# Performance work log

Measured on AMD Instinct MI355X. Metric: run time of the kernel, lower is better.

Reference implementation:

```python
import jax, jax.numpy as jnp
import numpy as np

D_MODEL = 512
HEADS = 8
D_FF = 1024
EPS = 1e-5


def layer_norm(x, gamma, beta):
    mu = jnp.mean(x, axis=-1, keepdims=True)
    var = jnp.mean(jnp.square(x - mu), axis=-1, keepdims=True)
    return (x - mu) * jax.lax.rsqrt(var + EPS) * gamma + beta


def mha(q, k, v, mask=None):
    # q,k,v: [B, S, D]; no input/output projections in the original module
    B, Sq, D = q.shape
    Sk = k.shape[1]
    dk = D // HEADS
    qh = q.reshape(B, Sq, HEADS, dk).transpose(0, 2, 1, 3)  # [B,H,Sq,dk]
    kh = k.reshape(B, Sk, HEADS, dk).transpose(0, 2, 1, 3)
    vh = v.reshape(B, Sk, HEADS, dk).transpose(0, 2, 1, 3)
    scores = jnp.einsum('bhqd,bhkd->bhqk', qh, kh) / np.sqrt(dk).astype(q.dtype)
    if mask is not None:
        scores = jnp.where(mask == 0, jnp.asarray(-1e9, scores.dtype), scores)
    attn = jax.nn.softmax(scores, axis=-1)  # dropout is identity in eval mode
    out = jnp.einsum('bhqk,bhkd->bhqd', attn, vh)
    return out.transpose(0, 2, 1, 3).reshape(B, Sq, D)


def setup_inputs() -> dict:
    key = jax.random.key(0)
    ks = jax.random.split(key, 8)
    B, S = 4, 2048
    x = jax.random.normal(ks[0], (B, S, D_MODEL), dtype=jnp.float32)
    encoder_output = jax.random.normal(ks[1], (B, S, D_MODEL), dtype=jnp.float32)
    mask = jax.random.randint(ks[2], (B, 1, S, S), 0, 2, dtype=jnp.int32)
    params = {
        'ln1_g': jnp.ones((D_MODEL,), jnp.float32), 'ln1_b': jnp.zeros((D_MODEL,), jnp.float32),
        'ln2_g': jnp.ones((D_MODEL,), jnp.float32), 'ln2_b': jnp.zeros((D_MODEL,), jnp.float32),
        'ln3_g': jnp.ones((D_MODEL,), jnp.float32), 'ln3_b': jnp.zeros((D_MODEL,), jnp.float32),
        'W1': jax.random.normal(ks[3], (D_MODEL, D_FF), jnp.float32) * (1.0 / np.sqrt(D_MODEL)),
        'b1': jnp.zeros((D_FF,), jnp.float32),
        'W2': jax.random.normal(ks[4], (D_FF, D_MODEL), jnp.float32) * (1.0 / np.sqrt(D_FF)),
        'b2': jnp.zeros((D_MODEL,), jnp.float32),
    }
    return {'x': x, 'encoder_output': encoder_output, 'mask': mask, **params}


def reference(x, encoder_output, mask, ln1_g, ln1_b, ln2_g, ln2_b, ln3_g, ln3_b, W1, b1, W2, b2):
    # pre-norm masked self-attention + residual (dropout = identity, eval mode)
    x1 = layer_norm(x, ln1_g, ln1_b)
    x = x + mha(x1, x1, x1, mask)
    # pre-norm cross-attention + residual
    x1 = layer_norm(x, ln2_g, ln2_b)
    x = x + mha(x1, encoder_output, encoder_output, None)
    # pre-norm FFN + residual
    x1 = layer_norm(x, ln3_g, ln3_b)
    h = jax.nn.relu(x1 @ W1 + b1)
    x = x + (h @ W2 + b2)
    return x
```

## Files before the change

### kernel.cpp

```cpp
#include <hip/hip_runtime.h>
#include <hip/hip_bf16.h>

#define D_MODEL 512
#define HEADS   8
#define DK      64
#define D_FF    1024
#define SEQ     2048
#define BATCH   4
#define NTOK    (BATCH*SEQ)
#define NELEM   (NTOK*D_MODEL)

#define QSCALE  0.18033688011112042f
#define MFIX    40.0f

typedef __attribute__((ext_vector_type(8))) short bf8_t;
typedef __attribute__((ext_vector_type(4))) float f4_t;

#define GLD16(gp, lp) __builtin_amdgcn_global_load_lds( \
    (const __attribute__((address_space(1))) void*)(gp), \
    (__attribute__((address_space(3))) void*)(lp), 16, 0, 0)

__device__ __forceinline__ float ldf(const void* p, size_t i, int f32) {
    return f32 ? ((const float*)p)[i] : __bfloat162float(((const __hip_bfloat16*)p)[i]);
}
__device__ __forceinline__ short f2bf(float f) {
    union { __hip_bfloat16 h; short s; } u; u.h = __float2bfloat16(f); return u.s;
}
__device__ __forceinline__ float bf2f(short s) {
    return __uint_as_float(((unsigned)(unsigned short)s) << 16);
}
__device__ __forceinline__ unsigned fbits(float f) { return __float_as_uint(f); }

__device__ __forceinline__ float fast_exp2(float x) {
    float r; asm("v_exp_f32 %0, %1" : "=v"(r) : "v"(x)); return r;
}

__global__ void detect_k(const uint4* __restrict__ w, int* __restrict__ flags) {
    __shared__ int found;
    if (threadIdx.x == 0) found = 0;
    __syncthreads();
    int hit = 0;
    for (int i = threadIdx.x; i < 4096; i += 256) {
        uint4 u = w[i];
        if (((u.x & 0x7F80u) == 0x7F80u) || ((u.y & 0x7F80u) == 0x7F80u) ||
            ((u.z & 0x7F80u) == 0x7F80u) || ((u.w & 0x7F80u) == 0x7F80u)) hit = 1;
    }
    if (hit) atomicOr(&found, 1);
    __syncthreads();
    if (threadIdx.x == 0) flags[0] = found ? 1 : 0;
}

__device__ __forceinline__ void transpose_body(const void* src, __hip_bfloat16* dst,
                                               int K, int N, int bxi, int byi, int f32,
                                               __hip_bfloat16 (*t)[33]) {
    int bx = bxi * 32, by = byi * 32;
    int tx = threadIdx.x & 31, ty = threadIdx.x >> 5;
    #pragma unroll
    for (int j = 0; j < 32; j += 8)
        t[ty + j][tx] = __float2bfloat16(ldf(src, (size_t)(by + ty + j) * N + bx + tx, f32));
    __syncthreads();
    #pragma unroll
    for (int j = 0; j < 32; j += 8)
        dst[(size_t)(bx + ty + j) * K + by + tx] = t[tx][ty + j];
}

__global__ __launch_bounds__(256)
void prep_k(const void* __restrict__ enc, const int* __restrict__ mask,
            const void* __restrict__ W1, const void* __restrict__ W2,
            const int* __restrict__ flagp,
            __hip_bfloat16* __restrict__ bufE, unsigned* __restrict__ mb,
            __hip_bfloat16* __restrict__ W1T, __hip_bfloat16* __restrict__ W2T) {
    __shared__ __hip_bfloat16 t[32][33];
    int f32 = *flagp;
    int bid = blockIdx.x;
    if (bid < 16384) {
        int i = bid * 256 + threadIdx.x;
        bufE[i] = __float2bfloat16(ldf(enc, i, f32));
    } else if (bid < 18432) {
        int row  = (bid - 16384) * 4 + (threadIdx.x >> 6);
        int lane = threadIdx.x & 63;
        const int* mr = mask + (size_t)row * SEQ;
        for (int it = 0; it < SEQ/64; it++) {
            unsigned long long bal = __ballot(mr[it*64 + lane] != 0);
            if (lane == 0)  mb[(size_t)row*(SEQ/32) + it*2]     = (unsigned)bal;
            if (lane == 32) mb[(size_t)row*(SEQ/32) + it*2 + 1] = (unsigned)(bal >> 32);
        }
    } else if (bid < 18944) {
        int lb = bid - 18432;
        transpose_body(W1, W1T, D_MODEL, D_FF, lb & 31, lb >> 5, f32, t);
    } else {
        int lb = bid - 18944;
        transpose_body(W2, W2T, D_FF, D_MODEL, lb & 15, lb >> 4, f32, t);
    }
}

__global__ __launch_bounds__(256)
void ln_first_k(const void* __restrict__ x, const void* __restrict__ g,
                const void* __restrict__ b, const int* __restrict__ flagp,
                float* __restrict__ xout, __hip_bfloat16* __restrict__ y) {
    int f32  = *flagp;
    int row  = blockIdx.x * 4 + (threadIdx.x >> 6);
    int lane = threadIdx.x & 63;
    size_t base = (size_t)row * D_MODEL;
    float v[8];
    float s = 0.f;
    #pragma unroll
    for (int i = 0; i < 8; i++) { v[i] = ldf(x, base + lane + i*64, f32); s += v[i]; }
    #pragma unroll
    for (int off = 32; off; off >>= 1) s += __shfl_xor(s, off);
    float mu = s * (1.f / D_MODEL);
    float ss = 0.f;
    #pragma unroll
    for (int i = 0; i < 8; i++) { float d = v[i] - mu; ss += d * d; }
    #pragma unroll
    for (int off = 32; off; off >>= 1) ss += __shfl_xor(ss, off);
    float rstd = rsqrtf(ss * (1.f / D_MODEL) + 1e-5f);
    #pragma unroll
    for (int i = 0; i < 8; i++) {
        int c = lane + i*64;
        xout[base + c] = v[i];
        y[base + c] = __float2bfloat16((v[i] - mu) * rstd * ldf(g, c, f32) + ldf(b, c, f32));
    }
}

__global__ __launch_bounds__(256)
void layernorm_k(const float* __restrict__ x, const void* __restrict__ g,
                 const void* __restrict__ b, const int* __restrict__ flagp,
                 __hip_bfloat16* __restrict__ y) {
    int f32  = *flagp;
    int row  = blockIdx.x * 4 + (threadIdx.x >> 6);
    int lane = threadIdx.x & 63;
    const float* xr = x + (size_t)row * D_MODEL;
    float v[8];
    float s = 0.f;
    #pragma unroll
    for (int i = 0; i < 8; i++) { v[i] = xr[lane + i*64]; s += v[i]; }
    #pragma unroll
    for (int off = 32; off; off >>= 1) s += __shfl_xor(s, off);
    float mu = s * (1.f / D_MODEL);
    float ss = 0.f;
    #pragma unroll
    for (int i = 0; i < 8; i++) { float d = v[i] - mu; ss += d * d; }
    #pragma unroll
    for (int off = 32; off; off >>= 1) ss += __shfl_xor(ss, off);
    float rstd = rsqrtf(ss * (1.f / D_MODEL) + 1e-5f);
    __hip_bfloat16* yr = y + (size_t)row * D_MODEL;
    #pragma unroll
    for (int i = 0; i < 8; i++) {
        int c = lane + i*64;
        yr[c] = __float2bfloat16((v[i] - mu) * rstd * ldf(g, c, f32) + ldf(b, c, f32));
    }
}

__device__ __forceinline__ bf8_t prescale_q(bf8_t q) {
    bf8_t r;
    #pragma unroll
    for (int j = 0; j < 8; j++) r[j] = f2bf(bf2f(q[j]) * QSCALE);
    return r;
}

template<bool HAS_MASK>
__global__ __launch_bounds__(256, 2)
void attn_mfma_k(const __hip_bfloat16* __restrict__ Q, const __hip_bfloat16* __restrict__ K,
                 const __hip_bfloat16* __restrict__ V, const unsigned* __restrict__ mbits,
                 float* __restrict__ Xout) {
    int bid = blockIdx.x;
    int qt = bid & 15;
    int h  = (bid >> 4) & 7;
    int b  = bid >> 7;
    int q0 = qt * 128;
    int tid  = threadIdx.x;
    int w    = tid >> 6;
    int lane = tid & 63;
    int c    = lane & 15;
    int quad = lane >> 4;

    __shared__ __hip_bfloat16 Kt[4][64 * 64];
    __shared__ __hip_bfloat16 VT[4][64 * 64];
    __shared__ __hip_bfloat16 Pb[4][2][16 * 64];

    bf8_t qf[2][2];
    #pragma unroll
    for (int g = 0; g < 2; g++) {
        const __hip_bfloat16* qrp = Q + ((size_t)(b*SEQ + q0 + 32*w + 16*g + c)) * D_MODEL + h*DK;
        qf[g][0] = prescale_q(*(const bf8_t*)(qrp + quad*8));
        qf[g][1] = prescale_q(*(const bf8_t*)(qrp + 32 + quad*8));
    }

    int kpo[4][2], vpo[4][2];
    #pragma unroll
    for (int t = 0; t < 4; t++)
        #pragma unroll
        for (int kh = 0; kh < 2; kh++) {
            int row = 16*t + c;
            kpo[t][kh] = (row*64 + (((4*kh + quad) ^ (row & 7)) * 8)) * 2;
            vpo[t][kh] = (row*64 + (((4*kh + quad) ^ (row & 7) ^ ((row >> 3) & 7)) * 8)) * 2;
        }

    int key0 = (tid >> 3) * 2, d0 = (tid & 7) * 8;
    int vtwo[8];
    #pragma unroll
    for (int j = 0; j < 8; j++) {
        int dk = d0 + j;
        int ch = (key0 >> 3) ^ (dk & 7) ^ ((dk >> 3) & 7);
        vtwo[j] = dk*128 + ch*16 + (key0 & 7)*2;
    }

    int krow[2], kc8[2];
    #pragma unroll
    for (int i = 0; i < 2; i++) {
        int idx = i*256 + tid;
        krow[i] = idx >> 3;
        kc8[i]  = ((idx & 7) ^ (krow[i] & 7)) * 8;
    }

    char* pbw[2] = { (char*)&Pb[w][0][0], (char*)&Pb[w][1][0] };
    int pwoff[4], proff[2];
    #pragma unroll
    for (int nt = 0; nt < 4; nt++)
        pwoff[nt] = c*128 + (((2*nt + (quad >> 1)) ^ (c & 7)) * 16) + (quad & 1)*8;
    #pragma unroll
    for (int kh = 0; kh < 2; kh++)
        proff[kh] = c*128 + (((4*kh + quad) ^ (c & 7)) * 16);

    const unsigned* mrp[2] = {nullptr, nullptr};
    if (HAS_MASK) {
        mrp[0] = mbits + (size_t)(b*SEQ + q0 + 32*w + c) * (SEQ/32);
        mrp[1] = mrp[0] + (size_t)16 * (SEQ/32);
    }
    int qsh = quad * 4;

    short onev = (c == 0) ? (short)0x3F80 : (short)0;
    bf8_t ones = {onev, onev, onev, onev, onev, onev, onev, onev};

    f4_t o[2][4];
    #pragma unroll
    for (int g = 0; g < 2; g++)
        #pragma unroll
        for (int mt = 0; mt < 4; mt++) o[g][mt] = (f4_t){0.f,0.f,0.f,0.f};
    f4_t l_acc[2] = {(f4_t){0.f,0.f,0.f,0.f}, (f4_t){0.f,0.f,0.f,0.f}};

    const size_t kvbase = (size_t)b * SEQ * D_MODEL + (size_t)h * DK;

    auto loadV = [&](int k0, bf8_t (&r0)[2], bf8_t (&r1)[2]) {
        #pragma unroll
        for (int t = 0; t < 2; t++) {
            const __hip_bfloat16* Vg = V + kvbase + (size_t)(k0 + t*64 + key0) * D_MODEL + d0;
            r0[t] = *(const bf8_t*)Vg;
            r1[t] = *(const bf8_t*)(Vg + D_MODEL);
        }
    };
    auto stageK = [&](int k0, int bufbase) {
        #pragma unroll
        for (int t = 0; t < 2; t++) {
            const __hip_bfloat16* Kg = K + kvbase + (size_t)(k0 + t*64) * D_MODEL;
            GLD16(Kg + (size_t)krow[0]*D_MODEL + kc8[0], (char*)&Kt[bufbase + t][0] + (w*64) * 16);
            GLD16(Kg + (size_t)krow[1]*D_MODEL + kc8[1], (char*)&Kt[bufbase + t][0] + (256 + w*64) * 16);
        }
    };
    auto writeV = [&](const bf8_t (&r0)[2], const bf8_t (&r1)[2], int bufbase) {
        #pragma unroll
        for (int t = 0; t < 2; t++) {
            const unsigned* v0u = (const unsigned*)&r0[t];
            const unsigned* v1u = (const unsigned*)&r1[t];
            char* vb = (char*)&VT[bufbase + t][0];
            #pragma unroll
            for (int dw = 0; dw < 4; dw++) {
                *(unsigned*)(vb + vtwo[2*dw])     = __builtin_amdgcn_perm(v1u[dw], v0u[dw], 0x05040100u);
                *(unsigned*)(vb + vtwo[2*dw + 1]) = __builtin_amdgcn_perm(v1u[dw], v0u[dw], 0x07060302u);
            }
        }
    };

    uint4 pm[2];
    if (HAS_MASK) { pm[0] = *(const uint4*)(mrp[0]); pm[1] = *(const uint4*)(mrp[1]); }
    bf8_t cv0[2], cv1[2];
    loadV(0, cv0, cv1);
    stageK(0, 0);
    writeV(cv0, cv1, 0);
    __syncthreads();

    for (int ph = 0; ph < SEQ/128; ph++) {
        int pb = (ph & 1) ? 2 : 0;
        int nb = pb ^ 2;

        uint4 nm[2];
        bf8_t nv0[2], nv1[2];
        if (ph < SEQ/128 - 1) {
            int kn = (ph + 1) * 128;
            if (HAS_MASK) {
                nm[0] = *(const uint4*)(mrp[0] + (kn >> 5));
                nm[1] = *(const uint4*)(mrp[1] + (kn >> 5));
            }
            loadV(kn, nv0, nv1);
            stageK(kn, nb);
        }

        #pragma unroll
        for (int t = 0; t < 2; t++) {
            const char* ktb = (const char*)&Kt[pb + t][0];
            const char* vtb = (const char*)&VT[pb + t][0];

            f4_t s[2][4];
            #pragma unroll
            for (int nt = 0; nt < 4; nt++) {
                s[0][nt] = (f4_t){-MFIX,-MFIX,-MFIX,-MFIX};
                s[1][nt] = (f4_t){-MFIX,-MFIX,-MFIX,-MFIX};
            }
            __builtin_amdgcn_s_setprio(1);
            #pragma unroll
            for (int nt = 0; nt < 4; nt++)
                #pragma unroll
                for (int kh = 0; kh < 2; kh++) {
                    bf8_t kf = *(const bf8_t*)(ktb + kpo[nt][kh]);
                    s[0][nt] = __builtin_amdgcn_mfma_f32_16x16x32_bf16(kf, qf[0][kh], s[0][nt], 0, 0, 0);
                    s[1][nt] = __builtin_amdgcn_mfma_f32_16x16x32_bf16(kf, qf[1][kh], s[1][nt], 0, 0, 0);
                }
            __builtin_amdgcn_s_setprio(0);

            #pragma unroll
            for (int g = 0; g < 2; g++) {
                unsigned wq0 = 0xffffffffu, wq1 = 0xffffffffu;
                if (HAS_MASK) {
                    wq0 = (t ? pm[g].z : pm[g].x) >> qsh;
                    wq1 = (t ? pm[g].w : pm[g].y) >> qsh;
                }
                #pragma unroll
                for (int nt = 0; nt < 4; nt++) {
                    #pragma unroll
                    for (int r = 0; r < 4; r++) {
                        float p = fast_exp2(s[g][nt][r]);
                        if (HAS_MASK) {
                            unsigned sel = (nt < 2) ? wq0 : wq1;
                            if (!((sel >> ((nt & 1)*16 + r)) & 1u)) p = 0.f;
                        }
                        s[g][nt][r] = p;
                    }
                    unsigned pk0 = __builtin_amdgcn_perm(fbits(s[g][nt][1]), fbits(s[g][nt][0]), 0x07060302u);
                    unsigned pk1 = __builtin_amdgcn_perm(fbits(s[g][nt][3]), fbits(s[g][nt][2]), 0x07060302u);
                    *(uint2*)(pbw[g] + pwoff[nt]) = make_uint2(pk0, pk1);
                }
            }

            __builtin_amdgcn_s_setprio(1);
            #pragma unroll
            for (int kh = 0; kh < 2; kh++) {
                bf8_t pfA = *(const bf8_t*)(pbw[0] + proff[kh]);
                bf8_t pfB = *(const bf8_t*)(pbw[1] + proff[kh]);
                l_acc[0] = __builtin_amdgcn_mfma_f32_16x16x32_bf16(ones, pfA, l_acc[0], 0, 0, 0);
                l_acc[1] = __builtin_amdgcn_mfma_f32_16x16x32_bf16(ones, pfB, l_acc[1], 0, 0, 0);
                #pragma unroll
                for (int mt = 0; mt < 4; mt++) {
                    bf8_t vf = *(const bf8_t*)(vtb + vpo[mt][kh]);
                    o[0][mt] = __builtin_amdgcn_mfma_f32_16x16x32_bf16(vf, pfA, o[0][mt], 0, 0, 0);
                    o[1][mt] = __builtin_amdgcn_mfma_f32_16x16x32_bf16(vf, pfB, o[1][mt], 0, 0, 0);
                }
            }
            __builtin_amdgcn_s_setprio(0);
        }

        if (ph < SEQ/128 - 1) {
            writeV(nv0, nv1, nb);
            if (HAS_MASK) { pm[0] = nm[0]; pm[1] = nm[1]; }
        }
        __syncthreads();
    }

    #pragma unroll
    for (int g = 0; g < 2; g++) {
        float lq = __shfl(l_acc[g][0], c);
        float il = 1.f / fmaxf(lq, 1e-35f);
        size_t rb = ((size_t)(b*SEQ + q0 + 32*w + 16*g + c)) * D_MODEL + h*DK;
        #pragma unroll
        for (int mt = 0; mt < 4; mt++) {
            float4* xp = (float4*)(Xout + rb + 16*mt + quad*4);
            float4 x4 = *xp;
            x4.x += o[g][mt][0] * il;
            x4.y += o[g][mt][1] * il;
            x4.z += o[g][mt][2] * il;
            x4.w += o[g][mt][3] * il;
            *xp = x4;
        }
    }
}

__global__ __launch_bounds__(256, 2)
void gemm_relu_k(const __hip_bfloat16* __restrict__ A, const __hip_bfloat16* __restrict__ BT,
                 const void* __restrict__ bias, const int* __restrict__ flagp,
                 __hip_bfloat16* __restrict__ C, int Ksz, int Nsz) {
    int f32 = *flagp;
    __shared__ __hip_bfloat16 As[128 * 64];
    __shared__ __hip_bfloat16 Bs[128 * 64];
    int tid  = threadIdx.x;
    int w    = tid >> 6;
    int c    = tid & 15;
    int quad = (tid >> 4) & 3;
    int wy = w >> 1, wx = w & 1;
    int r0 = blockIdx.y * 128, c0 = blockIdx.x * 128;

    f4_t acc[4][4];
    #pragma unroll
    for (int i = 0; i < 4; i++)
        #pragma unroll
        for (int j = 0; j < 4; j++) acc[i][j] = (f4_t){0.f,0.f,0.f,0.f};

    for (int k0 = 0; k0 < Ksz; k0 += 64) {
        __syncthreads();
        #pragma unroll
        for (int i = 0; i < 4; i++) {
            int idx = i*256 + tid;
            int row = idx >> 3, c8 = idx & 7;
            GLD16(A  + (size_t)(r0 + row) * Ksz + k0 + ((c8 ^ (row & 7)) * 8),
                  (char*)As + (size_t)(i*256 + w*64) * 16);
            GLD16(BT + (size_t)(c0 + row) * Ksz + k0 + ((c8 ^ (row & 7)) * 8),
                  (char*)Bs + (size_t)(i*256 + w*64) * 16);
        }
        __syncthreads();

        #pragma unroll
        for (int kh = 0; kh < 2; kh++) {
            bf8_t af[4], bf[4];
            #pragma unroll
            for (int mt = 0; mt < 4; mt++) {
                int row = wy*64 + mt*16 + c;
                af[mt] = *(const bf8_t*)&As[row*64 + (((kh*4 + quad) ^ (row & 7)) * 8)];
            }
            #pragma unroll
            for (int nt = 0; nt < 4; nt++) {
                int row = wx*64 + nt*16 + c;
                bf[nt] = *(const bf8_t*)&Bs[row*64 + (((kh*4 + quad) ^ (row & 7)) * 8)];
            }
            #pragma unroll
            for (int mt = 0; mt < 4; mt++)
                #pragma unroll
                for (int nt = 0; nt < 4; nt++)
                    acc[mt][nt] = __builtin_amdgcn_mfma_f32_16x16x32_bf16(af[mt], bf[nt], acc[mt][nt], 0, 0, 0);
        }
    }

    #pragma unroll
    for (int mt = 0; mt < 4; mt++)
        #pragma unroll
        for (int nt = 0; nt < 4; nt++) {
            int col = c0 + wx*64 + nt*16 + c;
            float bv = ldf(bias, col, f32);
            #pragma unroll
            for (int r = 0; r < 4; r++) {
                int m = r0 + wy*64 + mt*16 + quad*4 + r;
                C[(size_t)m * Nsz + col] = __float2bfloat16(fmaxf(acc[mt][nt][r] + bv, 0.f));
            }
        }
}

__global__ __launch_bounds__(256, 2)
void gemm_out_k(const __hip_bfloat16* __restrict__ A, const __hip_bfloat16* __restrict__ BT,
                const void* __restrict__ bias, const float* __restrict__ resid,
                const int* __restrict__ flagp, void* __restrict__ out, int Ksz, int Nsz) {
    int f32 = *flagp;
    __shared__ __hip_bfloat16 As[128 * 64];
    __shared__ __hip_bfloat16 Bs[64 * 64];
    int tid  = threadIdx.x;
    int w    = tid >> 6;
    int c    = tid & 15;
    int quad = (tid >> 4) & 3;
    int r0 = blockIdx.y * 128, c0 = blockIdx.x * 64;

    f4_t acc[2][4];
    #pragma unroll
    for (int i = 0; i < 2; i++)
        #pragma unroll
        for (int j = 0; j < 4; j++) acc[i][j] = (f4_t){0.f,0.f,0.f,0.f};

    for (int k0 = 0; k0 < Ksz; k0 += 64) {
        __syncthreads();
        #pragma unroll
        for (int i = 0; i < 4; i++) {
            int idx = i*256 + tid;
            int row = idx >> 3, c8 = idx & 7;
            GLD16(A + (size_t)(r0 + row) * Ksz + k0 + ((c8 ^ (row & 7)) * 8),
                  (char*)As + (size_t)(i*256 + w*64) * 16);
        }
        #pragma unroll
        for (int i = 0; i < 2; i++) {
            int idx = i*256 + tid;
            int row = idx >> 3, c8 = idx & 7;
            GLD16(BT + (size_t)(c0 + row) * Ksz + k0 + ((c8 ^ (row & 7)) * 8),
                  (char*)Bs + (size_t)(i*256 + w*64) * 16);
        }
        __syncthreads();

        #pragma unroll
        for (int kh = 0; kh < 2; kh++) {
            bf8_t af[2], bf[4];
            #pragma unroll
            for (int mt = 0; mt < 2; mt++) {
                int row = w*32 + mt*16 + c;
                af[mt] = *(const bf8_t*)&As[row*64 + (((kh*4 + quad) ^ (row & 7)) * 8)];
            }
            #pragma unroll
            for (int nt = 0; nt < 4; nt++) {
                int row = nt*16 + c;
                bf[nt] = *(const bf8_t*)&Bs[row*64 + (((kh*4 + quad) ^ (row & 7)) * 8)];
            }
            #pragma unroll
            for (int mt = 0; mt < 2; mt++)
                #pragma unroll
                for (int nt = 0; nt < 4; nt++)
                    acc[mt][nt] = __builtin_amdgcn_mfma_f32_16x16x32_bf16(af[mt], bf[nt], acc[mt][nt], 0, 0, 0);
        }
    }

    #pragma unroll
    for (int mt = 0; mt < 2; mt++)
        #pragma unroll
        for (int nt = 0; nt < 4; nt++) {
            int col = c0 + nt*16 + c;
            float bv = ldf(bias, col, f32);
            #pragma unroll
            for (int r = 0; r < 4; r++) {
                int m = r0 + w*32 + mt*16 + quad*4 + r;
                float v = acc[mt][nt][r] + bv + resid[(size_t)m * Nsz + col];
                if (f32) ((float*)out)[(size_t)m * Nsz + col] = v;
                else     ((__hip_bfloat16*)out)[(size_t)m * Nsz + col] = __float2bfloat16(v);
            }
        }
}

extern "C" void kernel_launch(void* const* d_in, const int* in_sizes, int n_in,
                              void* d_out, int out_size, void* d_ws, size_t ws_size,
                              hipStream_t stream) {
    const void* x    = d_in[0];
    const void* enc  = d_in[1];
    const int*  mask = (const int*)d_in[2];
    const void* ln1g = d_in[3];
    const void* ln1b = d_in[4];
    const void* ln2g = d_in[5];
    const void* ln2b = d_in[6];
    const void* ln3g = d_in[7];
    const void* ln3b = d_in[8];
    const void* W1   = d_in[9];
    const void* b1   = d_in[10];
    const void* W2   = d_in[11];
    const void* b2   = d_in[12];

    char* ws = (char*)d_ws;
    float*          bufX  = (float*)ws;
    __hip_bfloat16* bufQ  = (__hip_bfloat16*)(ws + (16u<<20));
    __hip_bfloat16* bufE  = (__hip_bfloat16*)(ws + (24u<<20));
    __hip_bfloat16* bufH  = (__hip_bfloat16*)(ws + (32u<<20));
    __hip_bfloat16* W1T   = (__hip_bfloat16*)(ws + (48u<<20));
    __hip_bfloat16* W2T   = (__hip_bfloat16*)(ws + (49u<<20));
    unsigned*       mbits = (unsigned*)(ws + (50u<<20));
    int*            flags = (int*)(ws + (52u<<20));

    dim3 blk(256);
    detect_k<<<1, blk, 0, stream>>>((const uint4*)x, flags);
    prep_k<<<19456, blk, 0, stream>>>(enc, mask, W1, W2, flags, bufE, mbits, W1T, W2T);

    ln_first_k<<<NTOK/4, blk, 0, stream>>>(x, ln1g, ln1b, flags, bufX, bufQ);
    attn_mfma_k<true><<<BATCH*HEADS*(SEQ/128), blk, 0, stream>>>(bufQ, bufQ, bufQ, mbits, bufX);
    layernorm_k<<<NTOK/4, blk, 0, stream>>>(bufX, ln2g, ln2b, flags, bufQ);
    attn_mfma_k<false><<<BATCH*HEADS*(SEQ/128), blk, 0, stream>>>(bufQ, bufE, bufE, nullptr, bufX);
    layernorm_k<<<NTOK/4, blk, 0, stream>>>(bufX, ln3g, ln3b, flags, bufQ);
    gemm_relu_k<<<dim3(D_FF/128, NTOK/128), blk, 0, stream>>>(bufQ, W1T, b1, flags, bufH, D_MODEL, D_FF);
    gemm_out_k<<<dim3(D_MODEL/64, NTOK/128), blk, 0, stream>>>(bufH, W2T, b2, bufX, flags, d_out, D_FF, D_MODEL);
}
```

Before: 343.0 us.

## Fold first layernorm into prep kernel, swizzle block order, double-buffer GEMM tiles

Moves the first layernorm into the preprocessing kernel as extra blocks, which removes one kernel launch. Remaps block indices in the attention kernels and both FFN GEMMs so neighbouring blocks are spread across the 8 XCDs, aiming for better L2 locality. The GEMMs now double-buffer their LDS tiles, so the next K-slice is fetched while the current one is computed. LDS use doubles, which may lower occupancy at the declared launch bounds.

```diff
diff --git a/kernel.cpp b/kernel.cpp
--- a/kernel.cpp
+++ b/kernel.cpp
@@ -67,9 +67,12 @@
 __global__ __launch_bounds__(256)
 void prep_k(const void* __restrict__ enc, const int* __restrict__ mask,
             const void* __restrict__ W1, const void* __restrict__ W2,
+            const void* __restrict__ x, const void* __restrict__ ln1g,
+            const void* __restrict__ ln1b,
             const int* __restrict__ flagp,
             __hip_bfloat16* __restrict__ bufE, unsigned* __restrict__ mb,
-            __hip_bfloat16* __restrict__ W1T, __hip_bfloat16* __restrict__ W2T) {
+            __hip_bfloat16* __restrict__ W1T, __hip_bfloat16* __restrict__ W2T,
+            float* __restrict__ bufX, __hip_bfloat16* __restrict__ bufQ) {
     __shared__ __hip_bfloat16 t[32][33];
     int f32 = *flagp;
     int bid = blockIdx.x;
@@ -88,38 +91,32 @@
     } else if (bid < 18944) {
         int lb = bid - 18432;
         transpose_body(W1, W1T, D_MODEL, D_FF, lb & 31, lb >> 5, f32, t);
-    } else {
+    } else if (bid < 19456) {
         int lb = bid - 18944;
         transpose_body(W2, W2T, D_FF, D_MODEL, lb & 15, lb >> 4, f32, t);
-    }
-}
-
-__global__ __launch_bounds__(256)
-void ln_first_k(const void* __restrict__ x, const void* __restrict__ g,
-                const void* __restrict__ b, const int* __restrict__ flagp,
-                float* __restrict__ xout, __hip_bfloat16* __restrict__ y) {
-    int f32  = *flagp;
-    int row  = blockIdx.x * 4 + (threadIdx.x >> 6);
-    int lane = threadIdx.x & 63;
-    size_t base = (size_t)row * D_MODEL;
-    float v[8];
-    float s = 0.f;
-    #pragma unroll
-    for (int i = 0; i < 8; i++) { v[i] = ldf(x, base + lane + i*64, f32); s += v[i]; }
-    #pragma unroll
-    for (int off = 32; off; off >>= 1) s += __shfl_xor(s, off);
-    float mu = s * (1.f / D_MODEL);
-    float ss = 0.f;
-    #pragma unroll
-    for (int i = 0; i < 8; i++) { float d = v[i] - mu; ss += d * d; }
-    #pragma unroll
-    for (int off = 32; off; off >>= 1) ss += __shfl_xor(ss, off);
-    float rstd = rsqrtf(ss * (1.f / D_MODEL) + 1e-5f);
-    #pragma unroll
-    for (int i = 0; i < 8; i++) {
-        int c = lane + i*64;
-        xout[base + c] = v[i];
-        y[base + c] = __float2bfloat16((v[i] - mu) * rstd * ldf(g, c, f32) + ldf(b, c, f32));
+    } else {
+        int row  = (bid - 19456) * 4 + (threadIdx.x >> 6);
+        int lane = threadIdx.x & 63;
+        size_t base = (size_t)row * D_MODEL;
+        float v[8];
+        float s = 0.f;
+        #pragma unroll
+        for (int i = 0; i < 8; i++) { v[i] = ldf(x, base + lane + i*64, f32); s += v[i]; }
+        #pragma unroll
+        for (int off = 32; off; off >>= 1) s += __shfl_xor(s, off);
+        float mu = s * (1.f / D_MODEL);
+        float ss = 0.f;
+        #pragma unroll
+        for (int i = 0; i < 8; i++) { float d = v[i] - mu; ss += d * d; }
+        #pragma unroll
+        for (int off = 32; off; off >>= 1) ss += __shfl_xor(ss, off);
+        float rstd = rsqrtf(ss * (1.f / D_MODEL) + 1e-5f);
+        #pragma unroll
+        for (int i = 0; i < 8; i++) {
+            int c = lane + i*64;
+            bufX[base + c] = v[i];
+            bufQ[base + c] = __float2bfloat16((v[i] - mu) * rstd * ldf(ln1g, c, f32) + ldf(ln1b, c, f32));
+        }
     }
 }
 
@@ -164,7 +161,8 @@
 void attn_mfma_k(const __hip_bfloat16* __restrict__ Q, const __hip_bfloat16* __restrict__ K,
                  const __hip_bfloat16* __restrict__ V, const unsigned* __restrict__ mbits,
                  float* __restrict__ Xout) {
-    int bid = blockIdx.x;
+    int bid0 = blockIdx.x;
+    int bid = ((bid0 & 7) << 6) | (bid0 >> 3);
     int qt = bid & 15;
     int h  = (bid >> 4) & 7;
     int b  = bid >> 7;
@@ -389,14 +387,16 @@
                  const void* __restrict__ bias, const int* __restrict__ flagp,
                  __hip_bfloat16* __restrict__ C, int Ksz, int Nsz) {
     int f32 = *flagp;
-    __shared__ __hip_bfloat16 As[128 * 64];
-    __shared__ __hip_bfloat16 Bs[128 * 64];
+    __shared__ __hip_bfloat16 As[2][128 * 64];
+    __shared__ __hip_bfloat16 Bs[2][128 * 64];
     int tid  = threadIdx.x;
     int w    = tid >> 6;
     int c    = tid & 15;
     int quad = (tid >> 4) & 3;
     int wy = w >> 1, wx = w & 1;
-    int r0 = blockIdx.y * 128, c0 = blockIdx.x * 128;
+    int lin = blockIdx.y * gridDim.x + blockIdx.x;
+    int swz = ((lin & 7) << 6) | (lin >> 3);
+    int r0 = (swz >> 3) * 128, c0 = (swz & 7) * 128;
 
     f4_t acc[4][4];
     #pragma unroll
@@ -404,18 +404,24 @@
         #pragma unroll
         for (int j = 0; j < 4; j++) acc[i][j] = (f4_t){0.f,0.f,0.f,0.f};
 
-    for (int k0 = 0; k0 < Ksz; k0 += 64) {
-        __syncthreads();
+    auto stage = [&](int k0, int bi) {
         #pragma unroll
         for (int i = 0; i < 4; i++) {
             int idx = i*256 + tid;
             int row = idx >> 3, c8 = idx & 7;
             GLD16(A  + (size_t)(r0 + row) * Ksz + k0 + ((c8 ^ (row & 7)) * 8),
-                  (char*)As + (size_t)(i*256 + w*64) * 16);
+                  (char*)&As[bi][0] + (size_t)(i*256 + w*64) * 16);
             GLD16(BT + (size_t)(c0 + row) * Ksz + k0 + ((c8 ^ (row & 7)) * 8),
-                  (char*)Bs + (size_t)(i*256 + w*64) * 16);
-        }
-        __syncthreads();
+                  (char*)&Bs[bi][0] + (size_t)(i*256 + w*64) * 16);
+        }
+    };
+
+    stage(0, 0);
+    __syncthreads();
+    int nk = Ksz >> 6;
+    for (int ks = 0; ks < nk; ks++) {
+        int bi = ks & 1;
+        if (ks + 1 < nk) stage((ks + 1) << 6, bi ^ 1);
 
         #pragma unroll
         for (int kh = 0; kh < 2; kh++) {
@@ -423,12 +429,12 @@
             #pragma unroll
             for (int mt = 0; mt < 4; mt++) {
                 int row = wy*64 + mt*16 + c;
-                af[mt] = *(const bf8_t*)&As[row*64 + (((kh*4 + quad) ^ (row & 7)) * 8)];
+                af[mt] = *(const bf8_t*)&As[bi][row*64 + (((kh*4 + quad) ^ (row & 7)) * 8)];
             }
             #pragma unroll
             for (int nt = 0; nt < 4; nt++) {
                 int row = wx*64 + nt*16 + c;
-                bf[nt] = *(const bf8_t*)&Bs[row*64 + (((kh*4 + quad) ^ (row & 7)) * 8)];
+                bf[nt] = *(const bf8_t*)&Bs[bi][row*64 + (((kh*4 + quad) ^ (row & 7)) * 8)];
             }
             #pragma unroll
             for (int mt = 0; mt < 4; mt++)
@@ -436,6 +442,7 @@
                 for (int nt = 0; nt < 4; nt++)
                     acc[mt][nt] = __builtin_amdgcn_mfma_f32_16x16x32_bf16(af[mt], bf[nt], acc[mt][nt], 0, 0, 0);
         }
+        __syncthreads();
     }
 
     #pragma unroll
@@ -457,13 +464,15 @@
                 const void* __restrict__ bias, const float* __restrict__ resid,
                 const int* __restrict__ flagp, void* __restrict__ out, int Ksz, int Nsz) {
     int f32 = *flagp;
-    __shared__ __hip_bfloat16 As[128 * 64];
-    __shared__ __hip_bfloat16 Bs[64 * 64];
+    __shared__ __hip_bfloat16 As[2][128 * 64];
+    __shared__ __hip_bfloat16 Bs[2][64 * 64];
     int tid  = threadIdx.x;
     int w    = tid >> 6;
     int c    = tid & 15;
     int quad = (tid >> 4) & 3;
-    int r0 = blockIdx.y * 128, c0 = blockIdx.x * 64;
+    int lin = blockIdx.y * gridDim.x + blockIdx.x;
+    int swz = ((lin & 7) << 6) | (lin >> 3);
+    int r0 = (swz >> 3) * 128, c0 = (swz & 7) * 64;
 
     f4_t acc[2][4];
     #pragma unroll
@@ -471,23 +480,29 @@
         #pragma unroll
         for (int j = 0; j < 4; j++) acc[i][j] = (f4_t){0.f,0.f,0.f,0.f};
 
-    for (int k0 = 0; k0 < Ksz; k0 += 64) {
-        __syncthreads();
+    auto stage = [&](int k0, int bi) {
         #pragma unroll
         for (int i = 0; i < 4; i++) {
             int idx = i*256 + tid;
             int row = idx >> 3, c8 = idx & 7;
             GLD16(A + (size_t)(r0 + row) * Ksz + k0 + ((c8 ^ (row & 7)) * 8),
-                  (char*)As + (size_t)(i*256 + w*64) * 16);
+                  (char*)&As[bi][0] + (size_t)(i*256 + w*64) * 16);
         }
         #pragma unroll
         for (int i = 0; i < 2; i++) {
             int idx = i*256 + tid;
             int row = idx >> 3, c8 = idx & 7;
             GLD16(BT + (size_t)(c0 + row) * Ksz + k0 + ((c8 ^ (row & 7)) * 8),
-                  (char*)Bs + (size_t)(i*256 + w*64) * 16);
-        }
-        __syncthreads();
+                  (char*)&Bs[bi][0] + (size_t)(i*256 + w*64) * 16);
+        }
+    };
+
+    stage(0, 0);
+    __syncthreads();
+    int nk = Ksz >> 6;
+    for (int ks = 0; ks < nk; ks++) {
+        int bi = ks & 1;
+        if (ks + 1 < nk) stage((ks + 1) << 6, bi ^ 1);
 
         #pragma unroll
         for (int kh = 0; kh < 2; kh++) {
@@ -495,12 +510,12 @@
             #pragma unroll
             for (int mt = 0; mt < 2; mt++) {
                 int row = w*32 + mt*16 + c;
-                af[mt] = *(const bf8_t*)&As[row*64 + (((kh*4 + quad) ^ (row & 7)) * 8)];
+                af[mt] = *(const bf8_t*)&As[bi][row*64 + (((kh*4 + quad) ^ (row & 7)) * 8)];
             }
             #pragma unroll
             for (int nt = 0; nt < 4; nt++) {
                 int row = nt*16 + c;
-                bf[nt] = *(const bf8_t*)&Bs[row*64 + (((kh*4 + quad) ^ (row & 7)) * 8)];
+                bf[nt] = *(const bf8_t*)&Bs[bi][row*64 + (((kh*4 + quad) ^ (row & 7)) * 8)];
             }
             #pragma unroll
             for (int mt = 0; mt < 2; mt++)
@@ -508,6 +523,7 @@
                 for (int nt = 0; nt < 4; nt++)
                     acc[mt][nt] = __builtin_amdgcn_mfma_f32_16x16x32_bf16(af[mt], bf[nt], acc[mt][nt], 0, 0, 0);
         }
+        __syncthreads();
     }
 
     #pragma unroll
@@ -555,9 +571,9 @@
 
     dim3 blk(256);
     detect_k<<<1, blk, 0, stream>>>((const uint4*)x, flags);
-    prep_k<<<19456, blk, 0, stream>>>(enc, mask, W1, W2, flags, bufE, mbits, W1T, W2T);
-
-    ln_first_k<<<NTOK/4, blk, 0, stream>>>(x, ln1g, ln1b, flags, bufX, bufQ);
+    prep_k<<<21504, blk, 0, stream>>>(enc, mask, W1, W2, x, ln1g, ln1b, flags,
+                                      bufE, mbits, W1T, W2T, bufX, bufQ);
+
     attn_mfma_k<true><<<BATCH*HEADS*(SEQ/128), blk, 0, stream>>>(bufQ, bufQ, bufQ, mbits, bufX);
     layernorm_k<<<NTOK/4, blk, 0, stream>>>(bufX, ln2g, ln2b, flags, bufQ);
     attn_mfma_k<false><<<BATCH*HEADS*(SEQ/128), blk, 0, stream>>>(bufQ, bufE, bufE, nullptr, bufX);
```

Measured after the change: 330.3 us (median of 2 runs). 1.04x faster.

## Fuse first layernorm into prep kernel, vectorize loads, remap attention blocks, batch QK MFMAs

Applied to the files above, without the earlier changes.

Merges the first layernorm into the prep kernel, removing one launch. The encoder conversion and all layernorms now use 8-wide vectorized loads and stores, and encoder conversion needs fewer blocks. Attention block IDs are remapped so that consecutive blocks spread across batch and head, likely for XCD/L2 locality. Both QK^T tiles of a phase are computed before softmax, which lengthens the MFMA burst at the cost of more live score registers.

```diff
diff --git a/kernel.cpp b/kernel.cpp
--- a/kernel.cpp
+++ b/kernel.cpp
@@ -67,17 +67,29 @@
 __global__ __launch_bounds__(256)
 void prep_k(const void* __restrict__ enc, const int* __restrict__ mask,
             const void* __restrict__ W1, const void* __restrict__ W2,
+            const void* __restrict__ x, const void* __restrict__ ln1g,
+            const void* __restrict__ ln1b,
             const int* __restrict__ flagp,
             __hip_bfloat16* __restrict__ bufE, unsigned* __restrict__ mb,
-            __hip_bfloat16* __restrict__ W1T, __hip_bfloat16* __restrict__ W2T) {
+            __hip_bfloat16* __restrict__ W1T, __hip_bfloat16* __restrict__ W2T,
+            float* __restrict__ bufX, __hip_bfloat16* __restrict__ bufQ) {
     __shared__ __hip_bfloat16 t[32][33];
     int f32 = *flagp;
     int bid = blockIdx.x;
-    if (bid < 16384) {
-        int i = bid * 256 + threadIdx.x;
-        bufE[i] = __float2bfloat16(ldf(enc, i, f32));
-    } else if (bid < 18432) {
-        int row  = (bid - 16384) * 4 + (threadIdx.x >> 6);
+    if (bid < 2048) {
+        size_t i0 = ((size_t)bid * 256 + threadIdx.x) * 8;
+        bf8_t o8;
+        if (f32) {
+            const float4* ep = (const float4*)((const float*)enc + i0);
+            float4 a = ep[0], b4 = ep[1];
+            o8[0]=f2bf(a.x);  o8[1]=f2bf(a.y);  o8[2]=f2bf(a.z);  o8[3]=f2bf(a.w);
+            o8[4]=f2bf(b4.x); o8[5]=f2bf(b4.y); o8[6]=f2bf(b4.z); o8[7]=f2bf(b4.w);
+        } else {
+            o8 = *(const bf8_t*)((const __hip_bfloat16*)enc + i0);
+        }
+        *(bf8_t*)(bufE + i0) = o8;
+    } else if (bid < 4096) {
+        int row  = (bid - 2048) * 4 + (threadIdx.x >> 6);
         int lane = threadIdx.x & 63;
         const int* mr = mask + (size_t)row * SEQ;
         for (int it = 0; it < SEQ/64; it++) {
@@ -85,41 +97,47 @@
             if (lane == 0)  mb[(size_t)row*(SEQ/32) + it*2]     = (unsigned)bal;
             if (lane == 32) mb[(size_t)row*(SEQ/32) + it*2 + 1] = (unsigned)(bal >> 32);
         }
-    } else if (bid < 18944) {
-        int lb = bid - 18432;
+    } else if (bid < 4608) {
+        int lb = bid - 4096;
         transpose_body(W1, W1T, D_MODEL, D_FF, lb & 31, lb >> 5, f32, t);
+    } else if (bid < 5120) {
+        int lb = bid - 4608;
+        transpose_body(W2, W2T, D_FF, D_MODEL, lb & 15, lb >> 4, f32, t);
     } else {
-        int lb = bid - 18944;
-        transpose_body(W2, W2T, D_FF, D_MODEL, lb & 15, lb >> 4, f32, t);
-    }
-}
-
-__global__ __launch_bounds__(256)
-void ln_first_k(const void* __restrict__ x, const void* __restrict__ g,
-                const void* __restrict__ b, const int* __restrict__ flagp,
-                float* __restrict__ xout, __hip_bfloat16* __restrict__ y) {
-    int f32  = *flagp;
-    int row  = blockIdx.x * 4 + (threadIdx.x >> 6);
-    int lane = threadIdx.x & 63;
-    size_t base = (size_t)row * D_MODEL;
-    float v[8];
-    float s = 0.f;
-    #pragma unroll
-    for (int i = 0; i < 8; i++) { v[i] = ldf(x, base + lane + i*64, f32); s += v[i]; }
-    #pragma unroll
-    for (int off = 32; off; off >>= 1) s += __shfl_xor(s, off);
-    float mu = s * (1.f / D_MODEL);
-    float ss = 0.f;
-    #pragma unroll
-    for (int i = 0; i < 8; i++) { float d = v[i] - mu; ss += d * d; }
-    #pragma unroll
-    for (int off = 32; off; off >>= 1) ss += __shfl_xor(ss, off);
-    float rstd = rsqrtf(ss * (1.f / D_MODEL) + 1e-5f);
-    #pragma unroll
-    for (int i = 0; i < 8; i++) {
-        int c = lane + i*64;
-        xout[base + c] = v[i];
-        y[base + c] = __float2bfloat16((v[i] - mu) * rstd * ldf(g, c, f32) + ldf(b, c, f32));
+        int row  = (bid - 5120) * 4 + (threadIdx.x >> 6);
+        int lane = threadIdx.x & 63;
+        int c0   = lane * 8;
+        size_t base = (size_t)row * D_MODEL;
+        float v[8];
+        if (f32) {
+            const float4* xp = (const float4*)((const float*)x + base + c0);
+            float4 a = xp[0], b4 = xp[1];
+            v[0]=a.x; v[1]=a.y; v[2]=a.z; v[3]=a.w;
+            v[4]=b4.x; v[5]=b4.y; v[6]=b4.z; v[7]=b4.w;
+        } else {
+            bf8_t x8 = *(const bf8_t*)((const __hip_bfloat16*)x + base + c0);
+            #pragma unroll
+            for (int j = 0; j < 8; j++) v[j] = bf2f(x8[j]);
+        }
+        float s = 0.f;
+        #pragma unroll
+        for (int i = 0; i < 8; i++) s += v[i];
+        #pragma unroll
+        for (int off = 32; off; off >>= 1) s += __shfl_xor(s, off);
+        float mu = s * (1.f / D_MODEL);
+        float ss = 0.f;
+        #pragma unroll
+        for (int i = 0; i < 8; i++) { float d = v[i] - mu; ss += d * d; }
+        #pragma unroll
+        for (int off = 32; off; off >>= 1) ss += __shfl_xor(ss, off);
+        float rstd = rsqrtf(ss * (1.f / D_MODEL) + 1e-5f);
+        *(float4*)(bufX + base + c0)     = make_float4(v[0], v[1], v[2], v[3]);
+        *(float4*)(bufX + base + c0 + 4) = make_float4(v[4], v[5], v[6], v[7]);
+        bf8_t q8;
+        #pragma unroll
+        for (int j = 0; j < 8; j++)
+            q8[j] = f2bf((v[j] - mu) * rstd * ldf(ln1g, c0 + j, f32) + ldf(ln1b, c0 + j, f32));
+        *(bf8_t*)(bufQ + base + c0) = q8;
     }
 }
 
@@ -130,11 +148,14 @@
     int f32  = *flagp;
     int row  = blockIdx.x * 4 + (threadIdx.x >> 6);
     int lane = threadIdx.x & 63;
+    int c0   = lane * 8;
     const float* xr = x + (size_t)row * D_MODEL;
-    float v[8];
+    const float4* xp = (const float4*)(xr + c0);
+    float4 a = xp[0], b4 = xp[1];
+    float v[8] = {a.x, a.y, a.z, a.w, b4.x, b4.y, b4.z, b4.w};
     float s = 0.f;
     #pragma unroll
-    for (int i = 0; i < 8; i++) { v[i] = xr[lane + i*64]; s += v[i]; }
+    for (int i = 0; i < 8; i++) s += v[i];
     #pragma unroll
     for (int off = 32; off; off >>= 1) s += __shfl_xor(s, off);
     float mu = s * (1.f / D_MODEL);
@@ -144,12 +165,11 @@
     #pragma unroll
     for (int off = 32; off; off >>= 1) ss += __shfl_xor(ss, off);
     float rstd = rsqrtf(ss * (1.f / D_MODEL) + 1e-5f);
-    __hip_bfloat16* yr = y + (size_t)row * D_MODEL;
-    #pragma unroll
-    for (int i = 0; i < 8; i++) {
-        int c = lane + i*64;
-        yr[c] = __float2bfloat16((v[i] - mu) * rstd * ldf(g, c, f32) + ldf(b, c, f32));
-    }
+    bf8_t y8;
+    #pragma unroll
+    for (int j = 0; j < 8; j++)
+        y8[j] = f2bf((v[j] - mu) * rstd * ldf(g, c0 + j, f32) + ldf(b, c0 + j, f32));
+    *(bf8_t*)(y + (size_t)row * D_MODEL + c0) = y8;
 }
 
 __device__ __forceinline__ bf8_t prescale_q(bf8_t q) {
@@ -164,7 +184,8 @@
 void attn_mfma_k(const __hip_bfloat16* __restrict__ Q, const __hip_bfloat16* __restrict__ K,
                  const __hip_bfloat16* __restrict__ V, const unsigned* __restrict__ mbits,
                  float* __restrict__ Xout) {
-    int bid = blockIdx.x;
+    int bid0 = blockIdx.x;
+    int bid = ((bid0 & 7) << 6) | (bid0 >> 3);
     int qt = bid & 15;
     int h  = (bid >> 4) & 7;
     int b  = bid >> 7;
@@ -296,27 +317,33 @@
             stageK(kn, nb);
         }
 
+        f4_t s[2][2][4];
+        #pragma unroll
+        for (int t = 0; t < 2; t++)
+            #pragma unroll
+            for (int g = 0; g < 2; g++)
+                #pragma unroll
+                for (int nt = 0; nt < 4; nt++)
+                    s[t][g][nt] = (f4_t){-MFIX,-MFIX,-MFIX,-MFIX};
+
+        __builtin_amdgcn_s_setprio(1);
         #pragma unroll
         for (int t = 0; t < 2; t++) {
             const char* ktb = (const char*)&Kt[pb + t][0];
-            const char* vtb = (const char*)&VT[pb + t][0];
-
-            f4_t s[2][4];
-            #pragma unroll
-            for (int nt = 0; nt < 4; nt++) {
-                s[0][nt] = (f4_t){-MFIX,-MFIX,-MFIX,-MFIX};
-                s[1][nt] = (f4_t){-MFIX,-MFIX,-MFIX,-MFIX};
-            }
-            __builtin_amdgcn_s_setprio(1);
             #pragma unroll
             for (int nt = 0; nt < 4; nt++)
                 #pragma unroll
                 for (int kh = 0; kh < 2; kh++) {
                     bf8_t kf = *(const bf8_t*)(ktb + kpo[nt][kh]);
-                    s[0][nt] = __builtin_amdgcn_mfma_f32_16x16x32_bf16(kf, qf[0][kh], s[0][nt], 0, 0, 0);
-                    s[1][nt] = __builtin_amdgcn_mfma_f32_16x16x32_bf16(kf, qf[1][kh], s[1][nt], 0, 0, 0);
+                    s[t][0][nt] = __builtin_amdgcn_mfma_f32_16x16x32_bf16(kf, qf[0][kh], s[t][0][nt], 0, 0, 0);
+                    s[t][1][nt] = __builtin_amdgcn_mfma_f32_16x16x32_bf16(kf, qf[1][kh], s[t][1][nt], 0, 0, 0);
                 }
-            __builtin_amdgcn_s_setprio(0);
+        }
+        __builtin_amdgcn_s_setprio(0);
+
+        #pragma unroll
+        for (int t = 0; t < 2; t++) {
+            const char* vtb = (const char*)&VT[pb + t][0];
 
             #pragma unroll
             for (int g = 0; g < 2; g++) {
@@ -329,15 +356,15 @@
                 for (int nt = 0; nt < 4; nt++) {
                     #pragma unroll
                     for (int r = 0; r < 4; r++) {
-                        float p = fast_exp2(s[g][nt][r]);
+                        float p = fast_exp2(s[t][g][nt][r]);
                         if (HAS_MASK) {
                             unsigned sel = (nt < 2) ? wq0 : wq1;
                             if (!((sel >> ((nt & 1)*16 + r)) & 1u)) p = 0.f;
                         }
-                        s[g][nt][r] = p;
+                        s[t][g][nt][r] = p;
                     }
-                    unsigned pk0 = __builtin_amdgcn_perm(fbits(s[g][nt][1]), fbits(s[g][nt][0]), 0x07060302u);
-                    unsigned pk1 = __builtin_amdgcn_perm(fbits(s[g][nt][3]), fbits(s[g][nt][2]), 0x07060302u);
+                    unsigned pk0 = __builtin_amdgcn_perm(fbits(s[t][g][nt][1]), fbits(s[t][g][nt][0]), 0x07060302u);
+                    unsigned pk1 = __builtin_amdgcn_perm(fbits(s[t][g][nt][3]), fbits(s[t][g][nt][2]), 0x07060302u);
                     *(uint2*)(pbw[g] + pwoff[nt]) = make_uint2(pk0, pk1);
                 }
             }
@@ -555,9 +582,9 @@
 
     dim3 blk(256);
     detect_k<<<1, blk, 0, stream>>>((const uint4*)x, flags);
-    prep_k<<<19456, blk, 0, stream>>>(enc, mask, W1, W2, flags, bufE, mbits, W1T, W2T);
-
-    ln_first_k<<<NTOK/4, blk, 0, stream>>>(x, ln1g, ln1b, flags, bufX, bufQ);
+    prep_k<<<7168, blk, 0, stream>>>(enc, mask, W1, W2, x, ln1g, ln1b, flags,
+                                     bufE, mbits, W1T, W2T, bufX, bufQ);
+
     attn_mfma_k<true><<<BATCH*HEADS*(SEQ/128), blk, 0, stream>>>(bufQ, bufQ, bufQ, mbits, bufX);
     layernorm_k<<<NTOK/4, blk, 0, stream>>>(bufX, ln2g, ln2b, flags, bufQ);
     attn_mfma_k<false><<<BATCH*HEADS*(SEQ/128), blk, 0, stream>>>(bufQ, bufE, bufE, nullptr, bufX);
```

After: 369.7 us. +7.8%, slower.
